# Performance work log

Measured on AMD Instinct MI355X. Metric: run time of the kernel, lower is better.

Reference implementation:

```python
import jax, jax.numpy as jnp
import numpy as np

N, C, A = 4096, 1000, 64


def setup_inputs() -> dict:
    key = jax.random.key(0)
    k1, k2, k3, k4, k5 = jax.random.split(key, 5)
    weight_m = jax.random.normal(k1, (C, A), dtype=jnp.float32)
    y = jax.random.normal(k2, (N, C), dtype=jnp.float32)
    features = jax.random.normal(k3, (N, A), dtype=jnp.float32)
    target_x = jax.random.randint(k4, (N,), 0, C)
    ratio = jnp.float32(0.5)
    final_conv = jax.random.normal(k5, (N, A, A), dtype=jnp.float32) * 0.1
    return {
        "weight_m": weight_m,
        "y": y,
        "features": features,
        "target_x": target_x,
        "ratio": ratio,
        "final_conv": final_conv,
        "class_num": C,
    }


def reference(weight_m, y, features, target_x, ratio, final_conv, class_num):
    # weight_m: (C, A); y: (N, C); features: (N, A) (only supplies N, A)
    # target_x: (N,) int labels; final_conv: (N, A, A); ratio: scalar
    Wk = weight_m[target_x]                       # (N, A)  gather of label row
    d = weight_m[None, :, :] - Wk[:, None, :]     # (N, C, A) = NxW_ij - NxW_kj

    # sigma1 = ||w_j||^2 - ||w_{y_n}||^2
    w2 = jnp.sum(weight_m * weight_m, axis=-1)    # (C,)
    sigma1 = w2[None, :] - w2[target_x][:, None]  # (N, C)

    # sigma2 = ratio * diag(d @ CV @ d^T), computed directly (no NxCxC matrix)
    t = jnp.einsum('nca,nab->ncb', d, final_conv)  # (N, C, A)
    sigma2 = ratio * jnp.sum(t * d, axis=-1)       # (N, C)

    logits = y + 0.5 * sigma2 + sigma1             # (N, C)

    # mean cross-entropy (nn.CrossEntropyLoss default)
    logp = jax.nn.log_softmax(logits, axis=-1)
    nll = -jnp.take_along_axis(logp, target_x[:, None], axis=1)[:, 0]
    loss = jnp.mean(nll)
    return loss, y
```

## Files before the change

kernel.cpp:

```cpp
#include <hip/hip_runtime.h>
#include <hip/hip_bf16.h>
#include <stdint.h>
#include <stddef.h>

#define N_    4096
#define C_    1000
#define CP    1024
#define A_    64
#define KPACK 2080
#define KCROSS (KPACK + 64)
#define KTOT  2176
#define KHALF 1088
#define MS    68

typedef __bf16 bf16_2 __attribute__((ext_vector_type(2)));
typedef __bf16 bf16_8 __attribute__((ext_vector_type(8)));
typedef float  f32_4  __attribute__((ext_vector_type(4)));

__device__ __forceinline__ void gl2lds16(const void* g, void* l) {
  __builtin_amdgcn_global_load_lds(
      (const __attribute__((address_space(1))) void*)g,
      (__attribute__((address_space(3))) void*)l, 16, 0, 0);
}

__device__ __forceinline__ void unpack_pair(int k, int& a, int& b) {
  a = (int)(0.5f * (129.0f - sqrtf((float)(16641 - 8 * k))));
  if (a < 0) a = 0;
  while ((a + 1) * (129 - (a + 1)) / 2 <= k) ++a;
  while (a * (129 - a) / 2 > k) --a;
  b = k - a * (129 - a) / 2 + a;
}

__global__ __launch_bounds__(256) void prep_all(
    const float* __restrict__ W, const int* __restrict__ tgt,
    const float* __restrict__ CV, __bf16* __restrict__ Bo,
    float* __restrict__ w2, __bf16* __restrict__ Aq, float* __restrict__ qn) {
  __shared__ float Ms[64 * MS];
  __shared__ float up[4 * 64];
  __shared__ float wk[64];
  __shared__ float us[64];
  int t = threadIdx.x;

  if (blockIdx.x < 1024) {
    int c = blockIdx.x;
    float* ws = Ms;
    if (t < 64) {
      float w = (c < C_) ? W[c * 64 + t] : 0.f;
      ws[t] = w;
      float s = w * w;
      for (int o = 32; o; o >>= 1) s += __shfl_down(s, o);
      if (t == 0 && c < C_) w2[c] = s;
    }
    __syncthreads();
    __bf16* row = Bo + (size_t)c * KTOT;
    for (int p = t; p < KPACK / 2; p += 256) {
      int k = 2 * p;
      int a0, b0, a1, b1;
      unpack_pair(k, a0, b0);
      if (b0 == 63) { a1 = a0 + 1; b1 = a1; } else { a1 = a0; b1 = b0 + 1; }
      bf16_2 v;
      v[0] = (__bf16)(ws[a0] * ws[b0]);
      v[1] = (__bf16)(ws[a1] * ws[b1]);
      *(bf16_2*)(row + k) = v;
    }
    if (t < 64) row[KPACK + t] = (__bf16)ws[t];
    if (t >= 64 && t < 96) row[KCROSS + (t - 64)] = (__bf16)0.f;
  } else {
    int n = blockIdx.x - 1024;
    int lbl = tgt[n];
    if (t < 64) wk[t] = W[lbl * 64 + t];
    const float4* M4 = (const float4*)(CV + (size_t)n * 4096);
    for (int j = 0; j < 4; ++j) {
      int i4 = t + j * 256;
      int r = i4 >> 4, c4 = (i4 & 15) << 2;
      *(float4*)&Ms[r * MS + c4] = M4[i4];
    }
    __syncthreads();
    {
      int a = t & 63, seg = t >> 6;
      float acc = 0.f;
      for (int b = seg * 16; b < seg * 16 + 16; ++b)
        acc += (Ms[a * MS + b] + Ms[b * MS + a]) * wk[b];
      up[seg * 64 + a] = acc;
    }
    __syncthreads();
    if (t < 64) {
      float u = up[t] + up[64 + t] + up[128 + t] + up[192 + t];
      us[t] = u;
      float p = wk[t] * u;
      for (int o = 32; o; o >>= 1) p += __shfl_down(p, o);
      if (t == 0) qn[n] = 0.5f * p;
    }
    __syncthreads();
    __bf16* row = Aq + (size_t)n * KTOT;
    for (int p = t; p < KPACK / 2; p += 256) {
      int k = 2 * p;
      int a0, b0, a1, b1;
      unpack_pair(k, a0, b0);
      if (b0 == 63) { a1 = a0 + 1; b1 = a1; } else { a1 = a0; b1 = b0 + 1; }
      bf16_2 v;
      v[0] = (__bf16)((a0 == b0) ? Ms[a0 * MS + a0]
                                 : (Ms[a0 * MS + b0] + Ms[b0 * MS + a0]));
      v[1] = (__bf16)((a1 == b1) ? Ms[a1 * MS + a1]
                                 : (Ms[a1 * MS + b1] + Ms[b1 * MS + a1]));
      *(bf16_2*)(row + k) = v;
    }
    if (t < 64) row[KPACK + t] = (__bf16)(-us[t]);
    if (t >= 64 && t < 96) row[KCROSS + (t - 64)] = (__bf16)0.f;
  }
}

#define BM 128
#define BN 128
#define BK 64
__global__ __launch_bounds__(256) void gemm_s(const __bf16* __restrict__ Aq,
                                              const __bf16* __restrict__ Bo,
                                              __bf16* __restrict__ Sbase) {
  __shared__ __bf16 As[BM * BK];
  __shared__ __bf16 Bs[BN * BK];
  int t = threadIdx.x;
  int lane = t & 63;
  int w = t >> 6;
  int wr = w & 1;
  int wc = w >> 1;
  int rowBase = blockIdx.x * BM;
  int colBase = blockIdx.y * BN;
  int kb = blockIdx.z * KHALF;
  __bf16* S = Sbase + (size_t)blockIdx.z * ((size_t)N_ * CP);

  f32_4 acc[4][4];
  for (int mi = 0; mi < 4; ++mi)
    for (int ni = 0; ni < 4; ++ni)
      acc[mi][ni] = (f32_4){0.f, 0.f, 0.f, 0.f};

  int m0 = lane & 15;
  int qsw = m0 & 7;

  for (int k0 = kb; k0 < kb + KHALF; k0 += BK) {
    __syncthreads();
    for (int r = 0; r < 4; ++r) {
      int ch = r * 256 + t;
      int row_p = ch >> 3, qp = ch & 7;
      int q_log = qp ^ (row_p & 7);
      const __bf16* g = Aq + (size_t)(rowBase + row_p) * KTOT + k0 + (q_log << 3);
      gl2lds16(g, As + ch * 8);
    }
    for (int r = 0; r < 4; ++r) {
      int ch = r * 256 + t;
      int row_p = ch >> 3, qp = ch & 7;
      int q_log = qp ^ (row_p & 7);
      const __bf16* g = Bo + (size_t)(colBase + row_p) * KTOT + k0 + (q_log << 3);
      gl2lds16(g, Bs + ch * 8);
    }
    __syncthreads();
    for (int kk = 0; kk < BK; kk += 32) {
      int qbase = (kk >> 3) + (lane >> 4);
      int qphys = qbase ^ qsw;
      bf16_8 af[4], bf[4];
      for (int mi = 0; mi < 4; ++mi)
        af[mi] = *(const bf16_8*)&As[(wr * 64 + mi * 16 + m0) * BK + (qphys << 3)];
      for (int ni = 0; ni < 4; ++ni)
        bf[ni] = *(const bf16_8*)&Bs[(wc * 64 + ni * 16 + m0) * BK + (qphys << 3)];
      for (int mi = 0; mi < 4; ++mi)
        for (int ni = 0; ni < 4; ++ni)
          acc[mi][ni] = __builtin_amdgcn_mfma_f32_16x16x32_bf16(af[mi], bf[ni], acc[mi][ni], 0, 0, 0);
    }
  }

  int ccol = lane & 15;
  int rrow = (lane >> 4) * 4;
  for (int mi = 0; mi < 4; ++mi)
    for (int ni = 0; ni < 4; ++ni) {
      int r0 = rowBase + wr * 64 + mi * 16 + rrow;
      int c0 = colBase + wc * 64 + ni * 16 + ccol;
      for (int j = 0; j < 4; ++j)
        S[(size_t)(r0 + j) * CP + c0] = (__bf16)acc[mi][ni][j];
    }
}

__global__ __launch_bounds__(256) void epilogue(
    const __bf16* __restrict__ Sb, const float* __restrict__ y,
    const float* __restrict__ w2, const float* __restrict__ qn,
    const int* __restrict__ tgt, const float* __restrict__ ratio_p,
    float* __restrict__ nll, float* __restrict__ outy) {
  int t = threadIdx.x, lane = t & 63, w = t >> 6;
  int n = blockIdx.x * 4 + w;
  float hr = 0.5f * (*ratio_p);
  int lbl = tgt[n];
  float q = qn[n];
  float w2k = w2[lbl];
  const bf16_8* S0 = (const bf16_8*)(Sb + (size_t)n * CP);
  const bf16_8* S1 = (const bf16_8*)(Sb + 1ull * N_ * CP + (size_t)n * CP);
  const float* yr = y + (size_t)n * C_;
  float* oy = outy + (size_t)n * C_;
  float l[16];
  float mx = -1e30f;
  for (int i = 0; i < 2; ++i) {
    int idx = i * 64 + lane;
    bf16_8 a0 = S0[idx], a1 = S1[idx];
    int c0 = idx * 8;
    for (int j = 0; j < 8; ++j) {
      int c = c0 + j;
      float v = -1e30f;
      if (c < C_) {
        float s = (float)a0[j] + (float)a1[j];
        v = yr[c] + (w2[c] - w2k) + hr * (s + q);
      }
      l[i * 8 + j] = v;
      mx = fmaxf(mx, v);
    }
  }
  for (int c = lane; c < C_; c += 64) oy[c] = yr[c];
  for (int o = 32; o; o >>= 1) mx = fmaxf(mx, __shfl_xor(mx, o));
  float se = 0.f, lt = 0.f;
  for (int i = 0; i < 2; ++i) {
    int c0 = (i * 64 + lane) * 8;
    for (int j = 0; j < 8; ++j) {
      float v = l[i * 8 + j];
      se += expf(v - mx);
      lt += (c0 + j == lbl) ? v : 0.f;
    }
  }
  for (int o = 32; o; o >>= 1) {
    se += __shfl_xor(se, o);
    lt += __shfl_xor(lt, o);
  }
  if (lane == 0) nll[n] = (mx + logf(se)) - lt;
}

__global__ void reduce_loss(const float* __restrict__ nll, float* __restrict__ out) {
  int t = threadIdx.x;
  float s = 0.f;
  for (int i = t; i < N_; i += 256) s += nll[i];
  for (int o = 32; o; o >>= 1) s += __shfl_down(s, o);
  __shared__ float r[4];
  if ((t & 63) == 0) r[t >> 6] = s;
  __syncthreads();
  if (t == 0) out[0] = (r[0] + r[1] + r[2] + r[3]) * (1.0f / (float)N_);
}

extern "C" void kernel_launch(void* const* d_in, const int* in_sizes, int n_in,
                              void* d_out, int out_size, void* d_ws, size_t ws_size,
                              hipStream_t stream) {
  const float* W     = (const float*)d_in[0];
  const float* y     = (const float*)d_in[1];
  const int*   tgt   = (const int*)d_in[3];
  const float* ratio = (const float*)d_in[4];
  const float* CV    = (const float*)d_in[5];

  char* ws = (char*)d_ws;
  size_t off = 0;
  __bf16* Aq = (__bf16*)(ws + off); off += (size_t)N_ * KTOT * sizeof(__bf16);
  __bf16* Bo = (__bf16*)(ws + off); off += (size_t)CP * KTOT * sizeof(__bf16);
  __bf16* S  = (__bf16*)(ws + off); off += 2ull * N_ * CP * sizeof(__bf16);
  float* w2  = (float*)(ws + off);  off += 4096;
  float* qn  = (float*)(ws + off);  off += (size_t)N_ * sizeof(float);
  float* nll = (float*)(ws + off);  off += (size_t)N_ * sizeof(float);

  float* out = (float*)d_out;

  prep_all<<<1024 + N_, 256, 0, stream>>>(W, tgt, CV, Bo, w2, Aq, qn);
  gemm_s<<<dim3(N_ / BM, CP / BN, 2), 256, 0, stream>>>(Aq, Bo, S);
  epilogue<<<N_ / 4, 256, 0, stream>>>(S, y, w2, qn, tgt, ratio, nll, out + 1);
  reduce_loss<<<1, 256, 0, stream>>>(nll, out);
}
```

Before: 172.9 us.

## Switch packed quadratic-form GEMM operands from bf16 to fp8

The packed pair-product operands (Aq from covariance, Bo from weight outer products) are now quantized to fp8 instead of bf16. The GEMM uses fp8 MFMA with a 128-byte K tile, and the K split is moved to 1152 so each half is a multiple of the tile. This halves operand memory traffic and LDS footprint per K element and uses the higher-throughput fp8 matrix instructions. The cost is much lower precision in the sigma2 term, which may hurt loss accuracy, especially since the u cross terms and products of weights are quantized to e4m3.

```diff
diff --git a/kernel.cpp b/kernel.cpp
--- a/kernel.cpp
+++ b/kernel.cpp
@@ -10,10 +10,9 @@
 #define KPACK 2080
 #define KCROSS (KPACK + 64)
 #define KTOT  2176
-#define KHALF 1088
+#define KSPLIT 1152
 #define MS    68
 
-typedef __bf16 bf16_2 __attribute__((ext_vector_type(2)));
 typedef __bf16 bf16_8 __attribute__((ext_vector_type(8)));
 typedef float  f32_4  __attribute__((ext_vector_type(4)));
 
@@ -21,6 +20,10 @@
   __builtin_amdgcn_global_load_lds(
       (const __attribute__((address_space(1))) void*)g,
       (__attribute__((address_space(3))) void*)l, 16, 0, 0);
+}
+
+__device__ __forceinline__ uint16_t pk_fp8(float a, float b) {
+  return (uint16_t)(__builtin_amdgcn_cvt_pk_fp8_f32(a, b, 0, false) & 0xffff);
 }
 
 __device__ __forceinline__ void unpack_pair(int k, int& a, int& b) {
@@ -33,8 +36,8 @@
 
 __global__ __launch_bounds__(256) void prep_all(
     const float* __restrict__ W, const int* __restrict__ tgt,
-    const float* __restrict__ CV, __bf16* __restrict__ Bo,
-    float* __restrict__ w2, __bf16* __restrict__ Aq, float* __restrict__ qn) {
+    const float* __restrict__ CV, uint8_t* __restrict__ Bo,
+    float* __restrict__ w2, uint8_t* __restrict__ Aq, float* __restrict__ qn) {
   __shared__ float Ms[64 * MS];
   __shared__ float up[4 * 64];
   __shared__ float wk[64];
@@ -52,19 +55,16 @@
       if (t == 0 && c < C_) w2[c] = s;
     }
     __syncthreads();
-    __bf16* row = Bo + (size_t)c * KTOT;
+    uint8_t* row = Bo + (size_t)c * KTOT;
     for (int p = t; p < KPACK / 2; p += 256) {
       int k = 2 * p;
       int a0, b0, a1, b1;
       unpack_pair(k, a0, b0);
       if (b0 == 63) { a1 = a0 + 1; b1 = a1; } else { a1 = a0; b1 = b0 + 1; }
-      bf16_2 v;
-      v[0] = (__bf16)(ws[a0] * ws[b0]);
-      v[1] = (__bf16)(ws[a1] * ws[b1]);
-      *(bf16_2*)(row + k) = v;
-    }
-    if (t < 64) row[KPACK + t] = (__bf16)ws[t];
-    if (t >= 64 && t < 96) row[KCROSS + (t - 64)] = (__bf16)0.f;
+      *(uint16_t*)(row + k) = pk_fp8(ws[a0] * ws[b0], ws[a1] * ws[b1]);
+    }
+    if (t < 32) *(uint16_t*)(row + KPACK + 2 * t) = pk_fp8(ws[2 * t], ws[2 * t + 1]);
+    if (t >= 32 && t < 48) *(uint16_t*)(row + KCROSS + 2 * (t - 32)) = 0;
   } else {
     int n = blockIdx.x - 1024;
     int lbl = tgt[n];
@@ -92,32 +92,29 @@
       if (t == 0) qn[n] = 0.5f * p;
     }
     __syncthreads();
-    __bf16* row = Aq + (size_t)n * KTOT;
+    uint8_t* row = Aq + (size_t)n * KTOT;
     for (int p = t; p < KPACK / 2; p += 256) {
       int k = 2 * p;
       int a0, b0, a1, b1;
       unpack_pair(k, a0, b0);
       if (b0 == 63) { a1 = a0 + 1; b1 = a1; } else { a1 = a0; b1 = b0 + 1; }
-      bf16_2 v;
-      v[0] = (__bf16)((a0 == b0) ? Ms[a0 * MS + a0]
-                                 : (Ms[a0 * MS + b0] + Ms[b0 * MS + a0]));
-      v[1] = (__bf16)((a1 == b1) ? Ms[a1 * MS + a1]
-                                 : (Ms[a1 * MS + b1] + Ms[b1 * MS + a1]));
-      *(bf16_2*)(row + k) = v;
-    }
-    if (t < 64) row[KPACK + t] = (__bf16)(-us[t]);
-    if (t >= 64 && t < 96) row[KCROSS + (t - 64)] = (__bf16)0.f;
+      float v0 = (a0 == b0) ? Ms[a0 * MS + a0] : (Ms[a0 * MS + b0] + Ms[b0 * MS + a0]);
+      float v1 = (a1 == b1) ? Ms[a1 * MS + a1] : (Ms[a1 * MS + b1] + Ms[b1 * MS + a1]);
+      *(uint16_t*)(row + k) = pk_fp8(v0, v1);
+    }
+    if (t < 32) *(uint16_t*)(row + KPACK + 2 * t) = pk_fp8(-us[2 * t], -us[2 * t + 1]);
+    if (t >= 32 && t < 48) *(uint16_t*)(row + KCROSS + 2 * (t - 32)) = 0;
   }
 }
 
 #define BM 128
 #define BN 128
-#define BK 64
-__global__ __launch_bounds__(256) void gemm_s(const __bf16* __restrict__ Aq,
-                                              const __bf16* __restrict__ Bo,
+#define BK 128
+__global__ __launch_bounds__(256) void gemm_s(const uint8_t* __restrict__ Aq,
+                                              const uint8_t* __restrict__ Bo,
                                               __bf16* __restrict__ Sbase) {
-  __shared__ __bf16 As[BM * BK];
-  __shared__ __bf16 Bs[BN * BK];
+  __shared__ uint8_t As[BM * BK];
+  __shared__ uint8_t Bs[BN * BK];
   int t = threadIdx.x;
   int lane = t & 63;
   int w = t >> 6;
@@ -125,7 +122,8 @@
   int wc = w >> 1;
   int rowBase = blockIdx.x * BM;
   int colBase = blockIdx.y * BN;
-  int kb = blockIdx.z * KHALF;
+  int kb = blockIdx.z ? KSPLIT : 0;
+  int ke = blockIdx.z ? KTOT : KSPLIT;
   __bf16* S = Sbase + (size_t)blockIdx.z * ((size_t)N_ * CP);
 
   f32_4 acc[4][4];
@@ -134,36 +132,38 @@
       acc[mi][ni] = (f32_4){0.f, 0.f, 0.f, 0.f};
 
   int m0 = lane & 15;
-  int qsw = m0 & 7;
-
-  for (int k0 = kb; k0 < kb + KHALF; k0 += BK) {
+  int q = lane >> 4;
+  int sw = m0 & 7;
+
+  for (int k0 = kb; k0 < ke; k0 += BK) {
     __syncthreads();
     for (int r = 0; r < 4; ++r) {
       int ch = r * 256 + t;
       int row_p = ch >> 3, qp = ch & 7;
       int q_log = qp ^ (row_p & 7);
-      const __bf16* g = Aq + (size_t)(rowBase + row_p) * KTOT + k0 + (q_log << 3);
-      gl2lds16(g, As + ch * 8);
+      const uint8_t* g = Aq + (size_t)(rowBase + row_p) * KTOT + k0 + (q_log << 4);
+      gl2lds16(g, As + ch * 16);
     }
     for (int r = 0; r < 4; ++r) {
       int ch = r * 256 + t;
       int row_p = ch >> 3, qp = ch & 7;
       int q_log = qp ^ (row_p & 7);
-      const __bf16* g = Bo + (size_t)(colBase + row_p) * KTOT + k0 + (q_log << 3);
-      gl2lds16(g, Bs + ch * 8);
-    }
-    __syncthreads();
-    for (int kk = 0; kk < BK; kk += 32) {
-      int qbase = (kk >> 3) + (lane >> 4);
-      int qphys = qbase ^ qsw;
-      bf16_8 af[4], bf[4];
+      const uint8_t* g = Bo + (size_t)(colBase + row_p) * KTOT + k0 + (q_log << 4);
+      gl2lds16(g, Bs + ch * 16);
+    }
+    __syncthreads();
+    for (int s = 0; s < 4; ++s) {
+      int c_log = 2 * s + (q >> 1);
+      int off = ((c_log ^ sw) << 4) + ((q & 1) << 3);
+      long af[4], bf[4];
       for (int mi = 0; mi < 4; ++mi)
-        af[mi] = *(const bf16_8*)&As[(wr * 64 + mi * 16 + m0) * BK + (qphys << 3)];
+        af[mi] = *(const long*)&As[(wr * 64 + mi * 16 + m0) * BK + off];
       for (int ni = 0; ni < 4; ++ni)
-        bf[ni] = *(const bf16_8*)&Bs[(wc * 64 + ni * 16 + m0) * BK + (qphys << 3)];
+        bf[ni] = *(const long*)&Bs[(wc * 64 + ni * 16 + m0) * BK + off];
       for (int mi = 0; mi < 4; ++mi)
         for (int ni = 0; ni < 4; ++ni)
-          acc[mi][ni] = __builtin_amdgcn_mfma_f32_16x16x32_bf16(af[mi], bf[ni], acc[mi][ni], 0, 0, 0);
+          acc[mi][ni] = __builtin_amdgcn_mfma_f32_16x16x32_fp8_fp8(
+              af[mi], bf[ni], acc[mi][ni], 0, 0, 0);
     }
   }
 
@@ -250,12 +250,12 @@
 
   char* ws = (char*)d_ws;
   size_t off = 0;
-  __bf16* Aq = (__bf16*)(ws + off); off += (size_t)N_ * KTOT * sizeof(__bf16);
-  __bf16* Bo = (__bf16*)(ws + off); off += (size_t)CP * KTOT * sizeof(__bf16);
-  __bf16* S  = (__bf16*)(ws + off); off += 2ull * N_ * CP * sizeof(__bf16);
-  float* w2  = (float*)(ws + off);  off += 4096;
-  float* qn  = (float*)(ws + off);  off += (size_t)N_ * sizeof(float);
-  float* nll = (float*)(ws + off);  off += (size_t)N_ * sizeof(float);
+  uint8_t* Aq = (uint8_t*)(ws + off); off += (size_t)N_ * KTOT;
+  uint8_t* Bo = (uint8_t*)(ws + off); off += (size_t)CP * KTOT;
+  __bf16* S   = (__bf16*)(ws + off);  off += 2ull * N_ * CP * sizeof(__bf16);
+  float* w2   = (float*)(ws + off);   off += 4096;
+  float* qn   = (float*)(ws + off);   off += (size_t)N_ * sizeof(float);
+  float* nll  = (float*)(ws + off);   off += (size_t)N_ * sizeof(float);
 
   float* out = (float*)d_out;
 
```

Result: faster. 165.8 us (-4.1%).
